# Performance work log

Hardware: AMD Instinct MI355X
Metric: run time of the kernel (lower is better)

Reference implementation:

```python
import jax, jax.numpy as jnp
import numpy as np

PTS_DIM = 2
LOSS_WEIGHT = 1.0


def setup_inputs() -> dict:
    key = jax.random.key(0)
    k1, k2 = jax.random.split(key)
    pred = jax.random.normal(k1, (8192, 128), dtype=jnp.float32)
    target = jax.random.normal(k2, (8192, 128), dtype=jnp.float32)
    return {"pred": pred, "target": target}


def reference(pred, target):
    # Chamfer-style L1 order loss, reduction='mean', weight=None, avg_factor=None.
    n = pred.shape[0]
    p = pred.reshape(n, -1, PTS_DIM)    # [N, P, 2]
    t = target.reshape(n, -1, PTS_DIM)  # [N, P, 2]
    # Pairwise per-coordinate L1 distances: [N, P, P, 2]
    dist_mat = jnp.abs(p[:, :, None, :] - t[:, None, :, :])
    dist_1 = dist_mat.min(axis=2)  # min over target points -> [N, P, 2]
    dist_2 = dist_mat.min(axis=1)  # min over pred points   -> [N, P, 2]
    loss = (dist_1 + dist_2) * 0.5
    loss = loss.reshape(n, -1)  # [N, P*2]
    num_pts = pred.shape[-1] // PTS_DIM
    # weighted_loss with weight=None, reduction='mean' -> plain mean
    return LOSS_WEIGHT * loss.mean() / num_pts
```

## Files before the change

### kernel.cpp

```cpp
#include <hip/hip_runtime.h>


#define BLOCK 1024
#define WPB (BLOCK / 64)
#define ROW_FLOATS 128
#define NCHUNK 32

typedef float vf4 __attribute__((ext_vector_type(4)));

__global__ __launch_bounds__(BLOCK)
void l1_order_partial_kernel(const float* __restrict__ pred,
                             const float* __restrict__ target,
                             float* __restrict__ partials) {
    __shared__ float wsum[WPB];

    const int t = threadIdx.x;
    const int lane = t & 63;
    const int w = t >> 6;

    int row = __builtin_amdgcn_readfirstlane(blockIdx.x * WPB + w);

    const float* __restrict__ rp = pred   + (size_t)row * ROW_FLOATS;
    const float* __restrict__ rt = target + (size_t)row * ROW_FLOATS;

    const float2 pi = ((const float2*)rp)[lane];
    const float2 ti = ((const float2*)rt)[lane];
    const vf4 piv = {pi.x, pi.y, pi.x, pi.y};
    const vf4 tiv = {ti.x, ti.y, ti.x, ti.y};

    float m1x = 1e30f, m1y = 1e30f;
    float m2x = 1e30f, m2y = 1e30f;

    const vf4* __restrict__ rt4 = (const vf4*)rt;
    const vf4* __restrict__ rp4 = (const vf4*)rp;

    #pragma unroll
    for (int c = 0; c < NCHUNK; ++c) {
        const vf4 dt = piv - rt4[c];
        const vf4 dp = tiv - rp4[c];
        m1x = fminf(fminf(fabsf(dt.x), fabsf(dt.z)), m1x);
        m1y = fminf(fminf(fabsf(dt.y), fabsf(dt.w)), m1y);
        m2x = fminf(fminf(fabsf(dp.x), fabsf(dp.z)), m2x);
        m2y = fminf(fminf(fabsf(dp.y), fabsf(dp.w)), m2y);
    }

    float v = (m1x + m1y) + (m2x + m2y);

    #pragma unroll
    for (int off = 32; off > 0; off >>= 1)
        v += __shfl_down(v, off);

    if (lane == 0) wsum[w] = v;
    __syncthreads();

    if (t == 0) {
        float s = 0.0f;
        #pragma unroll
        for (int i = 0; i < WPB; ++i) s += wsum[i];
        partials[blockIdx.x] = s;
    }
}

__global__ __launch_bounds__(512)
void l1_order_reduce_kernel(const float* __restrict__ partials,
                            float* __restrict__ out) {
    __shared__ float ssum[8];
    const int t = threadIdx.x;
    const int lane = t & 63;
    const int w = t >> 6;

    float v = partials[t];

    #pragma unroll
    for (int off = 32; off > 0; off >>= 1)
        v += __shfl_down(v, off);

    if (lane == 0) ssum[w] = v;
    __syncthreads();

    if (t == 0) {
        float s = 0.0f;
        #pragma unroll
        for (int i = 0; i < 8; ++i) s += ssum[i];
        out[0] = s * 7.450580596923828e-09f;
    }
}

extern "C" void kernel_launch(void* const* d_in, const int* in_sizes, int n_in,
                              void* d_out, int out_size, void* d_ws, size_t ws_size,
                              hipStream_t stream) {
    const float* pred   = (const float*)d_in[0];
    const float* target = (const float*)d_in[1];
    float* out = (float*)d_out;
    float* partials = (float*)d_ws;

    const int n_rows = in_sizes[0] / ROW_FLOATS;
    const int grid   = n_rows / WPB;

    l1_order_partial_kernel<<<grid, BLOCK, 0, stream>>>(pred, target, partials);
    l1_order_reduce_kernel<<<1, 512, 0, stream>>>(partials, out);
}
```

Measured before the change: 63.65 us.

## Fuse partial and final reduction into one cooperative kernel with grid sync

Replaces the two-kernel scheme (a per-block partial-sum kernel followed by a single-block reduce kernel) with one cooperative launch of 256 blocks. Each wavefront now processes two rows, and a grid-wide sync lets block 0 finish the final sum. This removes a second kernel launch and its inter-kernel gap. The cost is a grid barrier, halved parallelism per wave, and cooperative-launch overhead. The grid size is hardcoded to 256 rather than derived from the input.

```diff
diff --git a/kernel.cpp b/kernel.cpp
--- a/kernel.cpp
+++ b/kernel.cpp
@@ -1,56 +1,68 @@
 #include <hip/hip_runtime.h>
+#include <hip/hip_cooperative_groups.h>
 
 
+#define GRID 256
 #define BLOCK 1024
 #define WPB (BLOCK / 64)
+#define RPW 2
 #define ROW_FLOATS 128
 #define NCHUNK 32
 
 typedef float vf4 __attribute__((ext_vector_type(4)));
 
+namespace cg = cooperative_groups;
+
 __global__ __launch_bounds__(BLOCK)
-void l1_order_partial_kernel(const float* __restrict__ pred,
-                             const float* __restrict__ target,
-                             float* __restrict__ partials) {
+void l1_order_fused_kernel(const float* __restrict__ pred,
+                           const float* __restrict__ target,
+                           float* __restrict__ partials,
+                           float* __restrict__ out) {
     __shared__ float wsum[WPB];
 
     const int t = threadIdx.x;
     const int lane = t & 63;
     const int w = t >> 6;
 
-    int row = __builtin_amdgcn_readfirstlane(blockIdx.x * WPB + w);
+    float acc = 0.0f;
 
-    const float* __restrict__ rp = pred   + (size_t)row * ROW_FLOATS;
-    const float* __restrict__ rt = target + (size_t)row * ROW_FLOATS;
+    #pragma unroll 1
+    for (int r = 0; r < RPW; ++r) {
+        const int row = __builtin_amdgcn_readfirstlane(
+            (blockIdx.x * WPB + w) * RPW + r);
 
-    const float2 pi = ((const float2*)rp)[lane];
-    const float2 ti = ((const float2*)rt)[lane];
-    const vf4 piv = {pi.x, pi.y, pi.x, pi.y};
-    const vf4 tiv = {ti.x, ti.y, ti.x, ti.y};
+        const float* __restrict__ rp = pred   + (size_t)row * ROW_FLOATS;
+        const float* __restrict__ rt = target + (size_t)row * ROW_FLOATS;
 
-    float m1x = 1e30f, m1y = 1e30f;
-    float m2x = 1e30f, m2y = 1e30f;
+        const float2 pi = ((const float2*)rp)[lane];
+        const float2 ti = ((const float2*)rt)[lane];
+        const vf4 piv = {pi.x, pi.y, pi.x, pi.y};
+        const vf4 tiv = {ti.x, ti.y, ti.x, ti.y};
 
-    const vf4* __restrict__ rt4 = (const vf4*)rt;
-    const vf4* __restrict__ rp4 = (const vf4*)rp;
+        float m1x = 1e30f, m1y = 1e30f;
+        float m2x = 1e30f, m2y = 1e30f;
 
-    #pragma unroll
-    for (int c = 0; c < NCHUNK; ++c) {
-        const vf4 dt = piv - rt4[c];
-        const vf4 dp = tiv - rp4[c];
-        m1x = fminf(fminf(fabsf(dt.x), fabsf(dt.z)), m1x);
-        m1y = fminf(fminf(fabsf(dt.y), fabsf(dt.w)), m1y);
-        m2x = fminf(fminf(fabsf(dp.x), fabsf(dp.z)), m2x);
-        m2y = fminf(fminf(fabsf(dp.y), fabsf(dp.w)), m2y);
+        const vf4* __restrict__ rt4 = (const vf4*)rt;
+        const vf4* __restrict__ rp4 = (const vf4*)rp;
+
+        #pragma unroll
+        for (int c = 0; c < NCHUNK; ++c) {
+            const vf4 dt = piv - rt4[c];
+            const vf4 dp = tiv - rp4[c];
+            m1x = fminf(fminf(fabsf(dt.x), fabsf(dt.z)), m1x);
+            m1y = fminf(fminf(fabsf(dt.y), fabsf(dt.w)), m1y);
+            m2x = fminf(fminf(fabsf(dp.x), fabsf(dp.z)), m2x);
+            m2y = fminf(fminf(fabsf(dp.y), fabsf(dp.w)), m2y);
+        }
+
+        acc += (m1x + m1y) + (m2x + m2y);
     }
-
-    float v = (m1x + m1y) + (m2x + m2y);
 
     #pragma unroll
     for (int off = 32; off > 0; off >>= 1)
-        v += __shfl_down(v, off);
+        acc += __shfl_down(acc, off);
 
-    if (lane == 0) wsum[w] = v;
+    if (lane == 0) wsum[w] = acc;
     __syncthreads();
 
     if (t == 0) {
@@ -58,31 +70,27 @@
         #pragma unroll
         for (int i = 0; i < WPB; ++i) s += wsum[i];
         partials[blockIdx.x] = s;
+        __threadfence();
     }
-}
 
-__global__ __launch_bounds__(512)
-void l1_order_reduce_kernel(const float* __restrict__ partials,
-                            float* __restrict__ out) {
-    __shared__ float ssum[8];
-    const int t = threadIdx.x;
-    const int lane = t & 63;
-    const int w = t >> 6;
+    cg::this_grid().sync();
 
-    float v = partials[t];
+    if (blockIdx.x == 0) {
+        float p = (t < GRID) ? partials[t] : 0.0f;
 
-    #pragma unroll
-    for (int off = 32; off > 0; off >>= 1)
-        v += __shfl_down(v, off);
+        #pragma unroll
+        for (int off = 32; off > 0; off >>= 1)
+            p += __shfl_down(p, off);
 
-    if (lane == 0) ssum[w] = v;
-    __syncthreads();
+        if (lane == 0) wsum[w] = p;
+        __syncthreads();
 
-    if (t == 0) {
-        float s = 0.0f;
-        #pragma unroll
-        for (int i = 0; i < 8; ++i) s += ssum[i];
-        out[0] = s * 7.450580596923828e-09f;
+        if (t == 0) {
+            float s = 0.0f;
+            #pragma unroll
+            for (int i = 0; i < WPB; ++i) s += wsum[i];
+            out[0] = s * 7.450580596923828e-09f;
+        }
     }
 }
 
@@ -94,9 +102,7 @@
     float* out = (float*)d_out;
     float* partials = (float*)d_ws;
 
-    const int n_rows = in_sizes[0] / ROW_FLOATS;
-    const int grid   = n_rows / WPB;
-
-    l1_order_partial_kernel<<<grid, BLOCK, 0, stream>>>(pred, target, partials);
-    l1_order_reduce_kernel<<<1, 512, 0, stream>>>(partials, out);
+    void* args[] = {(void*)&pred, (void*)&target, (void*)&partials, (void*)&out};
+    hipLaunchCooperativeKernel((void*)l1_order_fused_kernel,
+                               dim3(GRID), dim3(BLOCK), args, 0, stream);
 }
```

New measurement: 105.2 us. +65.3%, slower.
